# Optimization experiments

Measured on AMD Instinct MI355X. Metric: run time of the kernel, lower is better.

The kernel has to match this reference:

```python
import jax, jax.numpy as jnp
import numpy as np

N, T, D, H = 4, 2048, 512, 8
HD = D // H  # head dim = split size


def setup_inputs() -> dict:
    key = jax.random.key(0)
    k1, k2, k3, k4 = jax.random.split(key, 4)
    scale = 1.0 / np.sqrt(D)
    return {
        "query": jax.random.normal(k1, (N, T, D), dtype=jnp.float32),
        "Wk": jax.random.normal(k2, (D, D), dtype=jnp.float32) * scale,
        "Wv": jax.random.normal(k3, (D, D), dtype=jnp.float32) * scale,
        "Wo": jax.random.normal(k4, (D, D), dtype=jnp.float32) * scale,
    }


def reference(query, Wk, Wv, Wo):
    # torch.nn.Linear(x) == x @ W.T (no bias)
    querys = query                              # [N, T, D]
    keys = query @ Wk.T + query                 # residual-added keys [N, T, D]
    values = query @ Wv.T                       # [N, T, D]

    # split along feature dim into H heads, stacked on a leading head axis
    def split_heads(x):
        # [N, T, D] -> [H, N, T, HD]
        return jnp.transpose(x.reshape(N, T, H, HD), (2, 0, 1, 3))

    q = split_heads(querys)
    k = split_heads(keys)
    v = split_heads(values)

    scores = jnp.einsum("hnqd,hnkd->hnqk", q, k) / np.sqrt(HD).astype(np.float32)
    scores = jax.nn.softmax(scores, axis=3)      # [H, N, Tq, Tk]
    out = jnp.einsum("hnqk,hnkd->hnqd", scores, v)

    # concat heads back along feature dim: [H, N, T, HD] -> [N, T, D]
    out = jnp.transpose(out, (1, 2, 0, 3)).reshape(N, T, D)
    out = out @ Wo.T
    return out
```

## Files before the change

### kernel.cpp

```cpp
#include <hip/hip_runtime.h>
#include <cstdint>
#include <cstddef>

#define NB 4
#define TS 2048
#define DM 512
#define HN 8
#define HD 64

typedef __attribute__((ext_vector_type(8))) short bf16x8;
typedef __attribute__((ext_vector_type(16))) float f32x16;
typedef __attribute__((ext_vector_type(4))) float f32x4;
typedef __attribute__((ext_vector_type(4))) short short4v;
typedef __attribute__((ext_vector_type(4))) unsigned u32x4;

static __device__ __forceinline__ short f2bf(float f) {
  unsigned u = __float_as_uint(f);
  unsigned r = (u + 0x7fffu + ((u >> 16) & 1u)) >> 16;
  return (short)r;
}

static __device__ __forceinline__ float bf2f(short s) {
  return __uint_as_float(((unsigned)(unsigned short)s) << 16);
}

static __device__ __forceinline__ unsigned cvtpk(float lo, float hi) {
  unsigned r;
  asm("v_cvt_pk_bf16_f32 %0, %1, %2" : "=v"(r) : "v"(lo), "v"(hi));
  return r;
}

static __device__ __forceinline__ void gload16(const void* g, void* l) {
  __builtin_amdgcn_global_load_lds(
      (const __attribute__((address_space(1))) void*)g,
      (__attribute__((address_space(3))) void*)l, 16, 0, 0);
}

#define WAIT_VM(N) asm volatile("s_waitcnt vmcnt(" #N ")" ::: "memory")
#define BAR() __builtin_amdgcn_s_barrier()

#define MFMA16(a, b, c) __builtin_amdgcn_mfma_f32_16x16x32_bf16((a), (b), (c), 0, 0, 0)
#define MFMA32(a, b, c) __builtin_amdgcn_mfma_f32_32x32x16_bf16((a), (b), (c), 0, 0, 0)

__global__ __launch_bounds__(256) void cast_all(const float* __restrict__ Q,
                                                const float* __restrict__ Wk,
                                                const float* __restrict__ Wv,
                                                const float* __restrict__ Wo,
                                                short* __restrict__ Qb,
                                                short* __restrict__ Wb) {
  int i = blockIdx.x * 256 + threadIdx.x;
  const int Q4 = (NB * TS * DM) / 4;
  const float* src;
  short* dst;
  int off;
  if (i < Q4) {
    src = Q; dst = Qb; off = i;
  } else {
    int j = i - Q4;
    int which = j >> 16;
    off = j & 65535;
    src = which == 0 ? Wk : (which == 1 ? Wv : Wo);
    dst = Wb + ((size_t)which << 18);
  }
  float4 v = reinterpret_cast<const float4*>(src)[off];
  short4v o;
  o.x = f2bf(v.x);
  o.y = f2bf(v.y);
  o.z = f2bf(v.z);
  o.w = f2bf(v.w);
  reinterpret_cast<short4v*>(dst)[off] = o;
}

template <int MODE>
__global__ __launch_bounds__(256) void gemm512(const short* __restrict__ A,
                                               const short* __restrict__ W0,
                                               const short* __restrict__ W1,
                                               const float* __restrict__ resid,
                                               void* __restrict__ out0,
                                               void* __restrict__ out1) {
  __shared__ alignas(16) short lA[2][128 * 32];
  __shared__ alignas(16) short lB[2][64 * 32];
  const int row0 = blockIdx.x * 128;
  const int col0 = blockIdx.y * 64;
  const int z = (MODE == 3) ? blockIdx.z : 0;
  const short* W = (MODE == 3 && z == 1) ? W1 : W0;
  const int tid = threadIdx.x;
  const int lane = tid & 63;
  const int wave = tid >> 6;
  const int wr = wave >> 1, wc = wave & 1;
  const int fr = lane & 15, fk = (lane >> 4) * 8;

  f32x4 acc[4][2];
  const f32x4 z4 = {0.f, 0.f, 0.f, 0.f};
#pragma unroll
  for (int m = 0; m < 4; ++m)
#pragma unroll
    for (int nn = 0; nn < 2; ++nn) acc[m][nn] = z4;

  const int sr = tid >> 2;
  const int sc8 = (tid & 3) * 8;

#define GSTAGE(buf, kt)                                                \
  do {                                                                 \
    gload16(&A[(size_t)(row0 + sr) * DM + (kt) + sc8],                 \
            (char*)&lA[(buf)][0] + (size_t)tid * 16);                  \
    gload16(&A[(size_t)(row0 + 64 + sr) * DM + (kt) + sc8],            \
            (char*)&lA[(buf)][0] + 4096 + (size_t)tid * 16);           \
    gload16(&W[(size_t)(col0 + sr) * DM + (kt) + sc8],                 \
            (char*)&lB[(buf)][0] + (size_t)tid * 16);                  \
  } while (0)

  GSTAGE(0, 0);
  int cur = 0;
  for (int kt = 0; kt < 16; ++kt) {
    if (kt < 15) {
      GSTAGE(cur ^ 1, (kt + 1) * 32);
      WAIT_VM(3);
    } else {
      WAIT_VM(0);
    }
    BAR();
    bf16x8 af[4], bfr[2];
#pragma unroll
    for (int m = 0; m < 4; ++m)
      af[m] = *reinterpret_cast<const bf16x8*>(&lA[cur][(wr * 64 + m * 16 + fr) * 32 + fk]);
#pragma unroll
    for (int nn = 0; nn < 2; ++nn)
      bfr[nn] = *reinterpret_cast<const bf16x8*>(&lB[cur][(wc * 32 + nn * 16 + fr) * 32 + fk]);
    __builtin_amdgcn_s_setprio(1);
#pragma unroll
    for (int m = 0; m < 4; ++m)
#pragma unroll
      for (int nn = 0; nn < 2; ++nn) acc[m][nn] = MFMA16(af[m], bfr[nn], acc[m][nn]);
    __builtin_amdgcn_s_setprio(0);
    BAR();
    cur ^= 1;
  }
#undef GSTAGE

#pragma unroll
  for (int m = 0; m < 4; ++m) {
#pragma unroll
    for (int nn = 0; nn < 2; ++nn) {
#pragma unroll
      for (int i = 0; i < 4; ++i) {
        int gr = row0 + wr * 64 + m * 16 + (lane >> 4) * 4 + i;
        int gc = col0 + wc * 32 + nn * 16 + fr;
        float v = acc[m][nn][i];
        if (MODE == 3) {
          if (z == 0) {
            v += resid[(size_t)gr * DM + gc];
            reinterpret_cast<short*>(out0)[(size_t)gr * DM + gc] = f2bf(v);
          } else {
            int nb = gr >> 11, t = gr & (TS - 1);
            int hh = gc >> 6, dd = gc & (HD - 1);
            reinterpret_cast<short*>(out1)[((size_t)(nb * HN + hh) * HD + dd) * TS + t] = f2bf(v);
          }
        } else {
          reinterpret_cast<float*>(out0)[(size_t)gr * DM + gc] = v;
        }
      }
    }
  }
}

__global__ __launch_bounds__(512, 4) void attn(const short* __restrict__ Qb,
                                               const short* __restrict__ Kb,
                                               const short* __restrict__ Vt,
                                               short* __restrict__ Ob) {
  __shared__ alignas(16) short kv[2][2][2][64 * 64];
  const int bid = blockIdx.x;
  const int blk = (bid & 7) * 64 + (bid >> 3);
  const int qt = blk & 15;
  const int nh = blk >> 4;
  const int h = nh & (HN - 1);
  const int n = nh >> 3;
  const int wv = threadIdx.x >> 6, lane = threadIdx.x & 63;
  const int grp = wv >> 2, qs = wv & 3;
  const int l31 = lane & 31, hf = lane >> 5;
  const int q0 = qt * 128 + qs * 32;
  const float SC2 = 0.18033688011f;

  bf16x8 qf[4];
  const short* qrow = Qb + (size_t)(n * TS + q0 + l31) * DM + h * HD;
#pragma unroll
  for (int ks = 0; ks < 4; ++ks) {
    bf16x8 t = *reinterpret_cast<const bf16x8*>(qrow + ks * 16 + hf * 8);
#pragma unroll
    for (int j = 0; j < 8; ++j) t[j] = f2bf(bf2f(t[j]) * SC2);
    qf[ks] = t;
  }

  bf16x8 ones;
#pragma unroll
  for (int i = 0; i < 8; ++i) ones[i] = (short)0x3F80;

  f32x16 o0, o1, osum;
#pragma unroll
  for (int r = 0; r < 16; ++r) {
    o0[r] = 0.f;
    o1[r] = 0.f;
    osum[r] = 0.f;
  }

  const int srow8 = lane >> 3;
  const int scol = ((lane & 7) ^ srow8) * 8;
  const int swz = (l31 & 7) << 4;
  const int tbase = grp * 16;

#define STAGE(buf, t)                                                       \
  do {                                                                      \
    int r0_ = qs * 16 + srow8;                                              \
    int r1_ = r0_ + 8;                                                      \
    char* kb_ = (char*)&kv[grp][(buf)][0][0] + qs * 2048;                   \
    char* vb_ = (char*)&kv[grp][(buf)][1][0] + qs * 2048;                   \
    gload16(Kb + (size_t)(n * TS + (t) * 64 + r0_) * DM + h * HD + scol, kb_);        \
    gload16(Kb + (size_t)(n * TS + (t) * 64 + r1_) * DM + h * HD + scol, kb_ + 1024); \
    gload16(Vt + ((size_t)(nh * HD + r0_) * TS + (t) * 64 + scol), vb_);              \
    gload16(Vt + ((size_t)(nh * HD + r1_) * TS + (t) * 64 + scol), vb_ + 1024);       \
  } while (0)

  STAGE(0, tbase);

  int cur = 0;
  for (int j = 0; j < 16; ++j) {
    if (j < 15) {
      STAGE(cur ^ 1, tbase + j + 1);
      WAIT_VM(4);
    } else {
      WAIT_VM(0);
    }
    BAR();

    const char* Kl = (const char*)&kv[grp][cur][0][0];
    const char* Vl = (const char*)&kv[grp][cur][1][0];

    f32x16 s0, s1;
#pragma unroll
    for (int r = 0; r < 16; ++r) {
      s0[r] = 0.f;
      s1[r] = 0.f;
    }
    __builtin_amdgcn_s_setprio(1);
#pragma unroll
    for (int ks = 0; ks < 4; ++ks) {
      int colb = ks * 32 + hf * 16;
      bf16x8 ka0 = *reinterpret_cast<const bf16x8*>(Kl + l31 * 128 + (colb ^ swz));
      bf16x8 ka1 = *reinterpret_cast<const bf16x8*>(Kl + (l31 + 32) * 128 + (colb ^ swz));
      s0 = MFMA32(ka0, qf[ks], s0);
      s1 = MFMA32(ka1, qf[ks], s1);
    }
    __builtin_amdgcn_s_setprio(0);

#pragma unroll
    for (int r = 0; r < 16; ++r) {
      s0[r] = __builtin_amdgcn_exp2f(s0[r]);
      s1[r] = __builtin_amdgcn_exp2f(s1[r]);
    }

    unsigned w0[4][2], w1[4][2];
#pragma unroll
    for (int c = 0; c < 4; ++c) {
      w0[c][0] = cvtpk(s0[4 * c], s0[4 * c + 1]);
      w0[c][1] = cvtpk(s0[4 * c + 2], s0[4 * c + 3]);
      w1[c][0] = cvtpk(s1[4 * c], s1[4 * c + 1]);
      w1[c][1] = cvtpk(s1[4 * c + 2], s1[4 * c + 3]);
    }

    __builtin_amdgcn_s_setprio(1);
#pragma unroll
    for (int ks = 0; ks < 4; ++ks) {
      const int ce = (ks & 1) * 2, co = ce + 1;
      unsigned a0 = (ks < 2) ? w0[ce][0] : w1[ce][0];
      unsigned a1 = (ks < 2) ? w0[ce][1] : w1[ce][1];
      unsigned b0 = (ks < 2) ? w0[co][0] : w1[co][0];
      unsigned b1 = (ks < 2) ? w0[co][1] : w1[co][1];
      unsigned a0s = (unsigned)__shfl_xor((int)a0, 32);
      unsigned a1s = (unsigned)__shfl_xor((int)a1, 32);
      unsigned b0s = (unsigned)__shfl_xor((int)b0, 32);
      unsigned b1s = (unsigned)__shfl_xor((int)b1, 32);
      u32x4 pw;
      pw.x = hf ? b0s : a0;
      pw.y = hf ? b1s : a1;
      pw.z = hf ? b0 : a0s;
      pw.w = hf ? b1 : a1s;
      bf16x8 pa = *reinterpret_cast<bf16x8*>(&pw);

      int colb = ks * 32 + hf * 16;
      bf16x8 v0 = *reinterpret_cast<const bf16x8*>(Vl + l31 * 128 + (colb ^ swz));
      bf16x8 v1 = *reinterpret_cast<const bf16x8*>(Vl + (l31 + 32) * 128 + (colb ^ swz));
      o0 = MFMA32(pa, v0, o0);
      o1 = MFMA32(pa, v1, o1);
      osum = MFMA32(pa, ones, osum);
    }
    __builtin_amdgcn_s_setprio(0);

    BAR();
    cur ^= 1;
  }
#undef STAGE

  float* sp = (float*)&kv[0][0][0][0];
  const int sbase = (qs * 64 + lane) * 49;
  if (grp == 1) {
#pragma unroll
    for (int r = 0; r < 16; ++r) {
      sp[sbase + r] = o0[r];
      sp[sbase + 16 + r] = o1[r];
      sp[sbase + 32 + r] = osum[r];
    }
  }
  __syncthreads();
  if (grp == 0) {
#pragma unroll
    for (int r = 0; r < 16; ++r) {
      o0[r] += sp[sbase + r];
      o1[r] += sp[sbase + 16 + r];
      osum[r] += sp[sbase + 32 + r];
    }
#pragma unroll
    for (int r = 0; r < 16; ++r) {
      int q = q0 + (r & 3) + 8 * (r >> 2) + 4 * hf;
      float is = 1.0f / osum[r];
      size_t base = (size_t)(n * TS + q) * DM + h * HD;
      Ob[base + l31] = f2bf(o0[r] * is);
      Ob[base + 32 + l31] = f2bf(o1[r] * is);
    }
  }
}

extern "C" void kernel_launch(void* const* d_in, const int* in_sizes, int n_in,
                              void* d_out, int out_size, void* d_ws, size_t ws_size,
                              hipStream_t stream) {
  (void)in_sizes; (void)n_in; (void)out_size; (void)ws_size;
  const float* Q = (const float*)d_in[0];
  const float* Wk = (const float*)d_in[1];
  const float* Wv = (const float*)d_in[2];
  const float* Wo = (const float*)d_in[3];

  const size_t QE = (size_t)NB * TS * DM;
  const size_t WE = (size_t)DM * DM;
  short* ws = (short*)d_ws;
  short* Qb = ws;
  short* Kb = Qb + QE;
  short* Vt = Kb + QE;
  short* Ao = Vt + QE;
  short* Wkb = Ao + QE;
  short* Wvb = Wkb + WE;
  short* Wob = Wvb + WE;

  {
    int total4 = (int)((QE + 3 * WE) / 4);
    cast_all<<<total4 / 256, 256, 0, stream>>>(Q, Wk, Wv, Wo, Qb, Wkb);
  }
  {
    dim3 g(64, 8, 2);
    gemm512<3><<<g, 256, 0, stream>>>(Qb, Wkb, Wvb, Q, (void*)Kb, (void*)Vt);
  }
  attn<<<NB * HN * (TS / 128), 512, 0, stream>>>(Qb, Kb, Vt, Ao);
  {
    dim3 g(64, 8, 1);
    gemm512<2><<<g, 256, 0, stream>>>(Ao, Wob, nullptr, nullptr, d_out, nullptr);
  }
}
```

Before: 94.73 us.

## Give each attention wave two query tiles and reuse K/V fragments

The attention kernel drops from 512 to 256 threads per block. Each wave now processes 64 query rows as two 32-row tiles, so every K and V fragment read from LDS feeds two sets of MFMAs. Staging is split so one wave of each pair loads K and the other loads V. The half-swap of the probability fragments uses v_permlane32_swap instead of shuffles plus selects. The QKV GEMM loop also replaces its explicit vmcnt wait and extra barrier with one __syncthreads per k-step. In exchange there are half as many waves per CU to hide latency, register pressure rises, and the end-of-loop reduction buffer grows.

```diff
diff --git a/kernel.cpp b/kernel.cpp
--- a/kernel.cpp
+++ b/kernel.cpp
@@ -28,6 +28,10 @@
   unsigned r;
   asm("v_cvt_pk_bf16_f32 %0, %1, %2" : "=v"(r) : "v"(lo), "v"(hi));
   return r;
+}
+
+static __device__ __forceinline__ void plane32swap(unsigned& x, unsigned& y) {
+  asm volatile("v_permlane32_swap_b32 %0, %1" : "+v"(x), "+v"(y));
 }
 
 static __device__ __forceinline__ void gload16(const void* g, void* l) {
@@ -111,15 +115,10 @@
   } while (0)
 
   GSTAGE(0, 0);
+  __syncthreads();
   int cur = 0;
   for (int kt = 0; kt < 16; ++kt) {
-    if (kt < 15) {
-      GSTAGE(cur ^ 1, (kt + 1) * 32);
-      WAIT_VM(3);
-    } else {
-      WAIT_VM(0);
-    }
-    BAR();
+    if (kt < 15) GSTAGE(cur ^ 1, (kt + 1) * 32);
     bf16x8 af[4], bfr[2];
 #pragma unroll
     for (int m = 0; m < 4; ++m)
@@ -133,7 +132,7 @@
 #pragma unroll
       for (int nn = 0; nn < 2; ++nn) acc[m][nn] = MFMA16(af[m], bfr[nn], acc[m][nn]);
     __builtin_amdgcn_s_setprio(0);
-    BAR();
+    __syncthreads();
     cur ^= 1;
   }
 #undef GSTAGE
@@ -164,7 +163,7 @@
   }
 }
 
-__global__ __launch_bounds__(512, 4) void attn(const short* __restrict__ Qb,
+__global__ __launch_bounds__(256, 2) void attn(const short* __restrict__ Qb,
                                                const short* __restrict__ Kb,
                                                const short* __restrict__ Vt,
                                                short* __restrict__ Ob) {
@@ -176,31 +175,33 @@
   const int h = nh & (HN - 1);
   const int n = nh >> 3;
   const int wv = threadIdx.x >> 6, lane = threadIdx.x & 63;
-  const int grp = wv >> 2, qs = wv & 3;
+  const int qw = wv & 1, grp = wv >> 1;
   const int l31 = lane & 31, hf = lane >> 5;
-  const int q0 = qt * 128 + qs * 32;
+  const int q0 = qt * 128 + qw * 64;
   const float SC2 = 0.18033688011f;
 
-  bf16x8 qf[4];
-  const short* qrow = Qb + (size_t)(n * TS + q0 + l31) * DM + h * HD;
-#pragma unroll
-  for (int ks = 0; ks < 4; ++ks) {
-    bf16x8 t = *reinterpret_cast<const bf16x8*>(qrow + ks * 16 + hf * 8);
-#pragma unroll
-    for (int j = 0; j < 8; ++j) t[j] = f2bf(bf2f(t[j]) * SC2);
-    qf[ks] = t;
+  bf16x8 qf[2][4];
+#pragma unroll
+  for (int qs = 0; qs < 2; ++qs) {
+    const short* qrow = Qb + (size_t)(n * TS + q0 + qs * 32 + l31) * DM + h * HD;
+#pragma unroll
+    for (int ks = 0; ks < 4; ++ks) {
+      bf16x8 t = *reinterpret_cast<const bf16x8*>(qrow + ks * 16 + hf * 8);
+#pragma unroll
+      for (int j = 0; j < 8; ++j) t[j] = f2bf(bf2f(t[j]) * SC2);
+      qf[qs][ks] = t;
+    }
   }
 
   bf16x8 ones;
 #pragma unroll
   for (int i = 0; i < 8; ++i) ones[i] = (short)0x3F80;
 
-  f32x16 o0, o1, osum;
+  f32x16 o00, o01, o10, o11, osum0, osum1;
 #pragma unroll
   for (int r = 0; r < 16; ++r) {
-    o0[r] = 0.f;
-    o1[r] = 0.f;
-    osum[r] = 0.f;
+    o00[r] = 0.f; o01[r] = 0.f; o10[r] = 0.f; o11[r] = 0.f;
+    osum0[r] = 0.f; osum1[r] = 0.f;
   }
 
   const int srow8 = lane >> 3;
@@ -208,16 +209,23 @@
   const int swz = (l31 & 7) << 4;
   const int tbase = grp * 16;
 
-#define STAGE(buf, t)                                                       \
-  do {                                                                      \
-    int r0_ = qs * 16 + srow8;                                              \
-    int r1_ = r0_ + 8;                                                      \
-    char* kb_ = (char*)&kv[grp][(buf)][0][0] + qs * 2048;                   \
-    char* vb_ = (char*)&kv[grp][(buf)][1][0] + qs * 2048;                   \
-    gload16(Kb + (size_t)(n * TS + (t) * 64 + r0_) * DM + h * HD + scol, kb_);        \
-    gload16(Kb + (size_t)(n * TS + (t) * 64 + r1_) * DM + h * HD + scol, kb_ + 1024); \
-    gload16(Vt + ((size_t)(nh * HD + r0_) * TS + (t) * 64 + scol), vb_);              \
-    gload16(Vt + ((size_t)(nh * HD + r1_) * TS + (t) * 64 + scol), vb_ + 1024);       \
+#define STAGE(buf, t)                                                            \
+  do {                                                                           \
+    if (qw == 0) {                                                               \
+      char* kb_ = (char*)&kv[grp][(buf)][0][0];                                  \
+      _Pragma("unroll") for (int rr = 0; rr < 8; ++rr) {                         \
+        int row_ = rr * 8 + srow8;                                               \
+        gload16(Kb + (size_t)(n * TS + (t) * 64 + row_) * DM + h * HD + scol,    \
+                kb_ + rr * 1024);                                                \
+      }                                                                          \
+    } else {                                                                     \
+      char* vb_ = (char*)&kv[grp][(buf)][1][0];                                  \
+      _Pragma("unroll") for (int rr = 0; rr < 8; ++rr) {                         \
+        int row_ = rr * 8 + srow8;                                               \
+        gload16(Vt + ((size_t)(nh * HD + row_) * TS + (t) * 64 + scol),          \
+                vb_ + rr * 1024);                                                \
+      }                                                                          \
+    }                                                                            \
   } while (0)
 
   STAGE(0, tbase);
@@ -226,7 +234,7 @@
   for (int j = 0; j < 16; ++j) {
     if (j < 15) {
       STAGE(cur ^ 1, tbase + j + 1);
-      WAIT_VM(4);
+      WAIT_VM(8);
     } else {
       WAIT_VM(0);
     }
@@ -235,63 +243,79 @@
     const char* Kl = (const char*)&kv[grp][cur][0][0];
     const char* Vl = (const char*)&kv[grp][cur][1][0];
 
-    f32x16 s0, s1;
-#pragma unroll
-    for (int r = 0; r < 16; ++r) {
-      s0[r] = 0.f;
-      s1[r] = 0.f;
-    }
-    __builtin_amdgcn_s_setprio(1);
+    bf16x8 kf[8];
 #pragma unroll
     for (int ks = 0; ks < 4; ++ks) {
       int colb = ks * 32 + hf * 16;
-      bf16x8 ka0 = *reinterpret_cast<const bf16x8*>(Kl + l31 * 128 + (colb ^ swz));
-      bf16x8 ka1 = *reinterpret_cast<const bf16x8*>(Kl + (l31 + 32) * 128 + (colb ^ swz));
-      s0 = MFMA32(ka0, qf[ks], s0);
-      s1 = MFMA32(ka1, qf[ks], s1);
-    }
-    __builtin_amdgcn_s_setprio(0);
-
-#pragma unroll
-    for (int r = 0; r < 16; ++r) {
-      s0[r] = __builtin_amdgcn_exp2f(s0[r]);
-      s1[r] = __builtin_amdgcn_exp2f(s1[r]);
-    }
-
-    unsigned w0[4][2], w1[4][2];
-#pragma unroll
-    for (int c = 0; c < 4; ++c) {
-      w0[c][0] = cvtpk(s0[4 * c], s0[4 * c + 1]);
-      w0[c][1] = cvtpk(s0[4 * c + 2], s0[4 * c + 3]);
-      w1[c][0] = cvtpk(s1[4 * c], s1[4 * c + 1]);
-      w1[c][1] = cvtpk(s1[4 * c + 2], s1[4 * c + 3]);
+      kf[ks] = *reinterpret_cast<const bf16x8*>(Kl + l31 * 128 + (colb ^ swz));
+      kf[ks + 4] = *reinterpret_cast<const bf16x8*>(Kl + (l31 + 32) * 128 + (colb ^ swz));
+    }
+
+    unsigned w0q[2][4][2], w1q[2][4][2];
+#pragma unroll
+    for (int qs = 0; qs < 2; ++qs) {
+      f32x16 s0, s1;
+#pragma unroll
+      for (int r = 0; r < 16; ++r) {
+        s0[r] = 0.f;
+        s1[r] = 0.f;
+      }
+      __builtin_amdgcn_s_setprio(1);
+#pragma unroll
+      for (int ks = 0; ks < 4; ++ks) {
+        s0 = MFMA32(kf[ks], qf[qs][ks], s0);
+        s1 = MFMA32(kf[ks + 4], qf[qs][ks], s1);
+      }
+      __builtin_amdgcn_s_setprio(0);
+#pragma unroll
+      for (int r = 0; r < 16; ++r) {
+        s0[r] = __builtin_amdgcn_exp2f(s0[r]);
+        s1[r] = __builtin_amdgcn_exp2f(s1[r]);
+      }
+#pragma unroll
+      for (int c = 0; c < 4; ++c) {
+        w0q[qs][c][0] = cvtpk(s0[4 * c], s0[4 * c + 1]);
+        w0q[qs][c][1] = cvtpk(s0[4 * c + 2], s0[4 * c + 3]);
+        w1q[qs][c][0] = cvtpk(s1[4 * c], s1[4 * c + 1]);
+        w1q[qs][c][1] = cvtpk(s1[4 * c + 2], s1[4 * c + 3]);
+      }
     }
 
     __builtin_amdgcn_s_setprio(1);
 #pragma unroll
     for (int ks = 0; ks < 4; ++ks) {
-      const int ce = (ks & 1) * 2, co = ce + 1;
-      unsigned a0 = (ks < 2) ? w0[ce][0] : w1[ce][0];
-      unsigned a1 = (ks < 2) ? w0[ce][1] : w1[ce][1];
-      unsigned b0 = (ks < 2) ? w0[co][0] : w1[co][0];
-      unsigned b1 = (ks < 2) ? w0[co][1] : w1[co][1];
-      unsigned a0s = (unsigned)__shfl_xor((int)a0, 32);
-      unsigned a1s = (unsigned)__shfl_xor((int)a1, 32);
-      unsigned b0s = (unsigned)__shfl_xor((int)b0, 32);
-      unsigned b1s = (unsigned)__shfl_xor((int)b1, 32);
-      u32x4 pw;
-      pw.x = hf ? b0s : a0;
-      pw.y = hf ? b1s : a1;
-      pw.z = hf ? b0 : a0s;
-      pw.w = hf ? b1 : a1s;
-      bf16x8 pa = *reinterpret_cast<bf16x8*>(&pw);
-
       int colb = ks * 32 + hf * 16;
       bf16x8 v0 = *reinterpret_cast<const bf16x8*>(Vl + l31 * 128 + (colb ^ swz));
       bf16x8 v1 = *reinterpret_cast<const bf16x8*>(Vl + (l31 + 32) * 128 + (colb ^ swz));
-      o0 = MFMA32(pa, v0, o0);
-      o1 = MFMA32(pa, v1, o1);
-      osum = MFMA32(pa, ones, osum);
+      const int ce = (ks & 1) * 2, co = ce + 1;
+      {
+        unsigned xa = (ks < 2) ? w0q[0][ce][0] : w1q[0][ce][0];
+        unsigned xb = (ks < 2) ? w0q[0][ce][1] : w1q[0][ce][1];
+        unsigned ya = (ks < 2) ? w0q[0][co][0] : w1q[0][co][0];
+        unsigned yb = (ks < 2) ? w0q[0][co][1] : w1q[0][co][1];
+        plane32swap(xa, ya);
+        plane32swap(xb, yb);
+        u32x4 pw;
+        pw.x = xa; pw.y = xb; pw.z = ya; pw.w = yb;
+        bf16x8 pa = *reinterpret_cast<bf16x8*>(&pw);
+        o00 = MFMA32(pa, v0, o00);
+        o01 = MFMA32(pa, v1, o01);
+        osum0 = MFMA32(pa, ones, osum0);
+      }
+      {
+        unsigned xa = (ks < 2) ? w0q[1][ce][0] : w1q[1][ce][0];
+        unsigned xb = (ks < 2) ? w0q[1][ce][1] : w1q[1][ce][1];
+        unsigned ya = (ks < 2) ? w0q[1][co][0] : w1q[1][co][0];
+        unsigned yb = (ks < 2) ? w0q[1][co][1] : w1q[1][co][1];
+        plane32swap(xa, ya);
+        plane32swap(xb, yb);
+        u32x4 pw;
+        pw.x = xa; pw.y = xb; pw.z = ya; pw.w = yb;
+        bf16x8 pa = *reinterpret_cast<bf16x8*>(&pw);
+        o10 = MFMA32(pa, v0, o10);
+        o11 = MFMA32(pa, v1, o11);
+        osum1 = MFMA32(pa, ones, osum1);
+      }
     }
     __builtin_amdgcn_s_setprio(0);
 
@@ -301,30 +325,47 @@
 #undef STAGE
 
   float* sp = (float*)&kv[0][0][0][0];
-  const int sbase = (qs * 64 + lane) * 49;
+  const int sbase = (int)(threadIdx.x & 127) * 97;
   if (grp == 1) {
 #pragma unroll
     for (int r = 0; r < 16; ++r) {
-      sp[sbase + r] = o0[r];
-      sp[sbase + 16 + r] = o1[r];
-      sp[sbase + 32 + r] = osum[r];
+      sp[sbase + r] = o00[r];
+      sp[sbase + 16 + r] = o01[r];
+      sp[sbase + 32 + r] = osum0[r];
+      sp[sbase + 48 + r] = o10[r];
+      sp[sbase + 64 + r] = o11[r];
+      sp[sbase + 80 + r] = osum1[r];
     }
   }
   __syncthreads();
   if (grp == 0) {
 #pragma unroll
     for (int r = 0; r < 16; ++r) {
-      o0[r] += sp[sbase + r];
-      o1[r] += sp[sbase + 16 + r];
-      osum[r] += sp[sbase + 32 + r];
+      o00[r] += sp[sbase + r];
+      o01[r] += sp[sbase + 16 + r];
+      osum0[r] += sp[sbase + 32 + r];
+      o10[r] += sp[sbase + 48 + r];
+      o11[r] += sp[sbase + 64 + r];
+      o11[r] += 0.f;
+      osum1[r] += sp[sbase + 80 + r];
     }
 #pragma unroll
     for (int r = 0; r < 16; ++r) {
-      int q = q0 + (r & 3) + 8 * (r >> 2) + 4 * hf;
-      float is = 1.0f / osum[r];
-      size_t base = (size_t)(n * TS + q) * DM + h * HD;
-      Ob[base + l31] = f2bf(o0[r] * is);
-      Ob[base + 32 + l31] = f2bf(o1[r] * is);
+      int crow = (r & 3) + 8 * (r >> 2) + 4 * hf;
+      {
+        int q = q0 + crow;
+        float is = 1.0f / osum0[r];
+        size_t base = (size_t)(n * TS + q) * DM + h * HD;
+        Ob[base + l31] = f2bf(o00[r] * is);
+        Ob[base + 32 + l31] = f2bf(o01[r] * is);
+      }
+      {
+        int q = q0 + 32 + crow;
+        float is = 1.0f / osum1[r];
+        size_t base = (size_t)(n * TS + q) * DM + h * HD;
+        Ob[base + l31] = f2bf(o10[r] * is);
+        Ob[base + 32 + l31] = f2bf(o11[r] * is);
+      }
     }
   }
 }
@@ -357,7 +398,7 @@
     dim3 g(64, 8, 2);
     gemm512<3><<<g, 256, 0, stream>>>(Qb, Wkb, Wvb, Q, (void*)Kb, (void*)Vt);
   }
-  attn<<<NB * HN * (TS / 128), 512, 0, stream>>>(Qb, Kb, Vt, Ao);
+  attn<<<NB * HN * (TS / 128), 256, 0, stream>>>(Qb, Kb, Vt, Ao);
   {
     dim3 g(64, 8, 1);
     gemm512<2><<<g, 256, 0, stream>>>(Ao, Wob, nullptr, nullptr, d_out, nullptr);
```

Result: faster. 92.24 us (-2.6%).
